# Optimization experiments

Measured on AMD Instinct MI355X. Metric: run time of the kernel, lower is better.

The kernel has to match this reference:

```python
import jax, jax.numpy as jnp
import numpy as np

EPS = 1e-5  # eqx.nn.LayerNorm default


def _layer_norm(x, w, b):
    m = x.mean(-1, keepdims=True)
    v = ((x - m) ** 2).mean(-1, keepdims=True)
    return (x - m) / jnp.sqrt(v + EPS) * w + b


def _s4_block(x, nw, nb, lre, lim, bre, bim, cre, cim, d, lstep, ow, ob, o2w, o2b):
    # x: [L, H]. One SequenceBlock: LayerNorm -> S4 recurrence (lax.scan) -> GELU -> GLU-style gated linear -> residual.
    skip = x
    h = _layer_norm(x, nw, nb)
    Lam = lre + 1j * lim                      # [H, N] complex diagonal state matrix
    step = jnp.exp(lstep)[:, None]            # [H, 1] per-channel timescale
    BL = 1.0 / (1.0 - (step / 2.0) * Lam)     # bilinear discretization
    Abar = BL * (1.0 + (step / 2.0) * Lam)    # [H, N]
    Bbar = BL * step * (bre + 1j * bim)       # [H, N]
    C = cre + 1j * cim                        # [H, N]

    def scan_fn(state, u):                    # state: [H, N] complex, u: [H]
        new = Abar * state + Bbar * u[:, None]
        y = 2.0 * jnp.sum(C * new, axis=-1).real + d * u
        return new, y

    init = jnp.zeros(Abar.shape, Abar.dtype)  # cell.init_state
    _, y = jax.lax.scan(scan_fn, init, h)     # [L, H]
    y = jax.nn.gelu(y)
    y = (y @ ow.T + ob) * jax.nn.sigmoid(y @ o2w.T + o2b)
    return skip + y


def setup_inputs() -> dict:
    key = jax.random.key(0)
    L, IN, OUT, H, N, NL = 2048, 4, 3, 512, 32, 4
    ks = jax.random.split(key, 16)
    return {
        "x": jax.random.normal(ks[0], (L, IN), jnp.float32),
        "enc_w": jax.random.normal(ks[1], (H, IN), jnp.float32) / np.sqrt(IN),
        "enc_b": jnp.zeros((H,), jnp.float32),
        "dec_w": jax.random.normal(ks[2], (OUT, H), jnp.float32) / np.sqrt(H),
        "dec_b": jnp.zeros((OUT,), jnp.float32),
        "norm_w": jnp.ones((NL, H), jnp.float32),
        "norm_b": jnp.zeros((NL, H), jnp.float32),
        "lam_re": -0.5 - jax.random.uniform(ks[3], (NL, H, N), jnp.float32),  # stable (Re < 0)
        "lam_im": np.pi * jax.random.normal(ks[4], (NL, H, N), jnp.float32),
        "b_re": jax.random.normal(ks[5], (NL, H, N), jnp.float32) / np.sqrt(N),
        "b_im": jax.random.normal(ks[6], (NL, H, N), jnp.float32) / np.sqrt(N),
        "c_re": jax.random.normal(ks[7], (NL, H, N), jnp.float32) / np.sqrt(N),
        "c_im": jax.random.normal(ks[8], (NL, H, N), jnp.float32) / np.sqrt(N),
        "d": jax.random.normal(ks[9], (NL, H), jnp.float32),
        "log_step": float(np.log(1e-3)) + float(np.log(1e-1) - np.log(1e-3)) * jax.random.uniform(ks[10], (NL, H), jnp.float32),
        "out_w": jax.random.normal(ks[11], (NL, H, H), jnp.float32) / np.sqrt(H),
        "out_b": jnp.zeros((NL, H), jnp.float32),
        "out2_w": jax.random.normal(ks[12], (NL, H, H), jnp.float32) / np.sqrt(H),
        "out2_b": jnp.zeros((NL, H), jnp.float32),
    }


def reference(x, enc_w, enc_b, dec_w, dec_b, norm_w, norm_b, lam_re, lam_im, b_re, b_im, c_re, c_im, d, log_step, out_w, out_b, out2_w, out2_b):
    h = x @ enc_w.T + enc_b                   # encoder: [L, IN] -> [L, H]
    for i in range(norm_w.shape[0]):          # fixed small n_layers loop
        h = _s4_block(h, norm_w[i], norm_b[i], lam_re[i], lam_im[i], b_re[i], b_im[i],
                      c_re[i], c_im[i], d[i], log_step[i], out_w[i], out_b[i], out2_w[i], out2_b[i])
    return h @ dec_w.T + dec_b                # decoder: [L, H] -> [L, OUT]
```

## Files before the change

### kernel.cpp

```cpp
#include <hip/hip_runtime.h>
#include <hip/hip_bf16.h>
#include <math.h>

#define LSEQ 2048
#define HD   512
#define NST  32
#define LC   32
#define NCHK 64
#define SUP  8
#define NSUP 8
#define HH   (HD * HD)

typedef __bf16 bf16;
typedef __bf16 bf16x8 __attribute__((ext_vector_type(8)));
typedef float  floatx4 __attribute__((ext_vector_type(4)));

__device__ __forceinline__ float wave_reduce_add(float v) {
#pragma unroll
    for (int m = 32; m; m >>= 1) v += __shfl_xor(v, m, 64);
    return v;
}

__device__ __forceinline__ float gelu_tanh(float x) {
    float z = 0.7978845608028654f * (x + 0.044715f * x * x * x);
    float e = __expf(2.f * z);
    float th = 1.f - 2.f / (e + 1.f);
    return 0.5f * x * (1.f + th);
}

__device__ __forceinline__ void make_ab(float lre, float lim, float step,
                                        float br0, float bi0,
                                        float& ar, float& ai, float& br, float& bi) {
    float s2 = 0.5f * step;
    float dr = 1.f - s2 * lre, di = -s2 * lim;
    float inv = 1.f / (dr * dr + di * di);
    float blr = dr * inv, bli = -di * inv;
    float nr = 1.f + s2 * lre, ni = s2 * lim;
    ar = blr * nr - bli * ni;
    ai = blr * ni + bli * nr;
    float tr = step * br0, ti = step * bi0;
    br = blr * tr - bli * ti;
    bi = blr * ti + bli * tr;
}

__global__ __launch_bounds__(256) void prep_kernel(
    const float* __restrict__ lre, const float* __restrict__ lim,
    const float* __restrict__ bre, const float* __restrict__ bim,
    const float* __restrict__ cre, const float* __restrict__ cim,
    const float* __restrict__ ls,
    float2* __restrict__ cA, float2* __restrict__ cB,
    float2* __restrict__ cC, float2* __restrict__ cAp) {
    int tid = blockIdx.x * 256 + threadIdx.x;
    int lay = tid >> 14, rem = tid & 16383;
    int ch = rem >> 5, n = rem & 31;
    int src = tid;
    float step = __expf(ls[lay * HD + ch]);
    float ar, ai, br, bi;
    make_ab(lre[src], lim[src], step, bre[src], bim[src], ar, ai, br, bi);
    float xr = ar, xi = ai;
#pragma unroll
    for (int q = 0; q < 5; ++q) { float tt = xr * xr - xi * xi; xi = 2.f * xr * xi; xr = tt; }
    int dst = (lay * NST + n) * HD + ch;
    cA[dst]  = make_float2(ar, ai);
    cB[dst]  = make_float2(br, bi);
    cC[dst]  = make_float2(2.f * cre[src], 2.f * cim[src]);
    cAp[dst] = make_float2(xr, xi);
}

__global__ __launch_bounds__(256) void cvt_kernel(
    const float* __restrict__ ow, const float* __restrict__ o2w,
    bf16* __restrict__ wb) {
    const float* src = blockIdx.y ? o2w : ow;
    bf16* dst = wb + blockIdx.y * (4 * HH);
    int i = (blockIdx.x * 256 + threadIdx.x) * 8;
    float4 a = *(const float4*)(src + i);
    float4 b = *(const float4*)(src + i + 4);
    bf16x8 o;
    o[0] = (bf16)a.x; o[1] = (bf16)a.y; o[2] = (bf16)a.z; o[3] = (bf16)a.w;
    o[4] = (bf16)b.x; o[5] = (bf16)b.y; o[6] = (bf16)b.z; o[7] = (bf16)b.w;
    *(bf16x8*)(dst + i) = o;
}

__global__ __launch_bounds__(256) void enc_kernel(
    const float* __restrict__ x, const float* __restrict__ w,
    const float* __restrict__ b, float* __restrict__ h) {
    int idx = blockIdx.x * 256 + threadIdx.x;
    int t = idx >> 9, i = idx & (HD - 1);
    float acc = b[i];
    float4 xv = *(const float4*)(x + t * 4);
    float4 wv = *(const float4*)(w + i * 4);
    acc = fmaf(xv.x, wv.x, acc);
    acc = fmaf(xv.y, wv.y, acc);
    acc = fmaf(xv.z, wv.z, acc);
    acc = fmaf(xv.w, wv.w, acc);
    h[idx] = acc;
}

__global__ __launch_bounds__(256) void ln_kernel(
    const float* __restrict__ h, float* __restrict__ hn,
    const float* __restrict__ w, const float* __restrict__ b) {
    int wv = threadIdx.x >> 6, lane = threadIdx.x & 63;
    int row = blockIdx.x * 4 + wv;
    const float* hp = h + row * HD + lane * 8;
    float v[8];
    *(float4*)(v)     = *(const float4*)(hp);
    *(float4*)(v + 4) = *(const float4*)(hp + 4);
    float s = 0.f;
#pragma unroll
    for (int e = 0; e < 8; ++e) s += v[e];
    s = wave_reduce_add(s);
    float m = s * (1.f / HD);
    float q = 0.f;
#pragma unroll
    for (int e = 0; e < 8; ++e) { float d = v[e] - m; q += d * d; }
    q = wave_reduce_add(q);
    float rstd = rsqrtf(q * (1.f / HD) + 1e-5f);
    float w8[8], b8[8];
    *(float4*)(w8)     = *(const float4*)(w + lane * 8);
    *(float4*)(w8 + 4) = *(const float4*)(w + lane * 8 + 4);
    *(float4*)(b8)     = *(const float4*)(b + lane * 8);
    *(float4*)(b8 + 4) = *(const float4*)(b + lane * 8 + 4);
    float o[8];
#pragma unroll
    for (int e = 0; e < 8; ++e)
        o[e] = (v[e] - m) * rstd * w8[e] + b8[e];
    float* op = hn + row * HD + lane * 8;
    *(float4*)op       = *(float4*)o;
    *(float4*)(op + 4) = *(float4*)(o + 4);
}

__global__ __launch_bounds__(256, 2) void p1_kernel(
    const float* __restrict__ u,
    const float2* __restrict__ cA, const float2* __restrict__ cB,
    float2* __restrict__ f, int lay) {
    __shared__ float tile[4 * LC * 16];
    int tid = threadIdx.x;
    int lane = tid & 63, w = tid >> 6;
    int chl = lane & 15;
    int ch = blockIdx.x * 16 + chl;
    int sub = lane >> 4;
    int chunk = blockIdx.y * 4 + w;
    int t0 = blockIdx.y * 4 * LC;
    const float* ub = u + (size_t)t0 * HD + blockIdx.x * 16;
#pragma unroll
    for (int r = 0; r < 8; ++r) {
        int idx = r * 256 + tid;
        tile[idx] = ub[(idx >> 4) * HD + (idx & 15)];
    }
    int cbase = (lay * NST + sub * 8) * HD + ch;
    float aR[8], aI[8], bR[8], bI[8];
#pragma unroll
    for (int j = 0; j < 8; ++j) {
        float2 t = cA[cbase + j * HD]; aR[j] = t.x; aI[j] = t.y;
        t = cB[cbase + j * HD];        bR[j] = t.x; bI[j] = t.y;
    }
    float sr[8], si[8];
#pragma unroll
    for (int j = 0; j < 8; ++j) { sr[j] = 0.f; si[j] = 0.f; }
    __syncthreads();
    const float* tp = tile + (w * LC) * 16 + chl;
#pragma unroll 4
    for (int t = 0; t < LC; ++t) {
        float uu = tp[t * 16];
#pragma unroll
        for (int j = 0; j < 8; ++j) {
            float nr = fmaf(aR[j], sr[j], fmaf(-aI[j], si[j], bR[j] * uu));
            float ni = fmaf(aI[j], sr[j], fmaf( aR[j], si[j], bI[j] * uu));
            sr[j] = nr; si[j] = ni;
        }
    }
    float2* fp = f + (chunk * NST + sub * 8) * HD + ch;
#pragma unroll
    for (int j = 0; j < 8; ++j) fp[j * HD] = make_float2(sr[j], si[j]);
}

__global__ __launch_bounds__(256) void p2a_kernel(
    float2* __restrict__ f, const float2* __restrict__ cAp, int lay) {
    int tg = blockIdx.x * 256 + threadIdx.x;
    int ch = tg & 511;
    int ns = tg >> 9;
    int n = ns & 31, sup = ns >> 5;
    float2 ap = cAp[(lay * NST + n) * HD + ch];
    float2* fp = f + ((sup * SUP) * NST + n) * HD + ch;
    float sr = 0.f, si = 0.f;
#pragma unroll
    for (int j = 0; j < SUP; ++j) {
        float2 v = fp[(size_t)j * NST * HD];
        float nr = fmaf(ap.x, sr, fmaf(-ap.y, si, v.x));
        float ni = fmaf(ap.y, sr, fmaf( ap.x, si, v.y));
        sr = nr; si = ni;
        fp[(size_t)j * NST * HD] = make_float2(sr, si);
    }
}

__global__ __launch_bounds__(256) void p2b_kernel(
    float2* __restrict__ f, const float2* __restrict__ cAp, int lay) {
    int tg = blockIdx.x * 256 + threadIdx.x;
    int ch = tg & 511, n = tg >> 9;
    float2 ap = cAp[(lay * NST + n) * HD + ch];
    float xr = ap.x, xi = ap.y;
#pragma unroll
    for (int q = 0; q < 3; ++q) { float tt = xr * xr - xi * xi; xi = 2.f * xr * xi; xr = tt; }
    float2* fp = f + ((SUP - 1) * NST + n) * HD + ch;
    const size_t stride = (size_t)SUP * NST * HD;
    float sr = 0.f, si = 0.f;
#pragma unroll
    for (int k = 0; k < NSUP; ++k) {
        float2 v = fp[k * stride];
        float nr = fmaf(xr, sr, fmaf(-xi, si, v.x));
        float ni = fmaf(xi, sr, fmaf( xr, si, v.y));
        sr = nr; si = ni;
        fp[k * stride] = make_float2(sr, si);
    }
}

__global__ __launch_bounds__(256) void p2c_kernel(
    float2* __restrict__ f, const float2* __restrict__ cAp, int lay) {
    int tg = blockIdx.x * 256 + threadIdx.x;
    int ch = tg & 511;
    int ns = tg >> 9;
    int n = ns & 31, sup = ns >> 5;
    if (sup == 0) return;
    float2 ap = cAp[(lay * NST + n) * HD + ch];
    float2 S = f[((sup * SUP - 1) * NST + n) * HD + ch];
    float2* fp = f + ((sup * SUP) * NST + n) * HD + ch;
    float wr = ap.x, wi = ap.y;
#pragma unroll
    for (int j = 0; j < SUP - 1; ++j) {
        float2 v = fp[(size_t)j * NST * HD];
        v.x += wr * S.x - wi * S.y;
        v.y += wr * S.y + wi * S.x;
        fp[(size_t)j * NST * HD] = v;
        float nwr = wr * ap.x - wi * ap.y;
        float nwi = wr * ap.y + wi * ap.x;
        wr = nwr; wi = nwi;
    }
}

__global__ __launch_bounds__(256, 2) void p3_kernel(
    const float* __restrict__ u, const float2* __restrict__ f,
    const float2* __restrict__ cA, const float2* __restrict__ cB,
    const float2* __restrict__ cC, const float* __restrict__ d_p,
    bf16* __restrict__ g, int lay) {
    __shared__ float tile[4 * LC * 16];
    int tid = threadIdx.x;
    int lane = tid & 63, w = tid >> 6;
    int chl = lane & 15;
    int ch = blockIdx.x * 16 + chl;
    int sub = lane >> 4;
    int chunk = blockIdx.y * 4 + w;
    int t0 = blockIdx.y * 4 * LC;
    const float* ub = u + (size_t)t0 * HD + blockIdx.x * 16;
#pragma unroll
    for (int r = 0; r < 8; ++r) {
        int idx = r * 256 + tid;
        tile[idx] = ub[(idx >> 4) * HD + (idx & 15)];
    }
    int cbase = (lay * NST + sub * 8) * HD + ch;
    float aR[8], aI[8], bR[8], bI[8], cR[8], cI[8];
#pragma unroll
    for (int j = 0; j < 8; ++j) {
        float2 t = cA[cbase + j * HD]; aR[j] = t.x; aI[j] = t.y;
        t = cB[cbase + j * HD];        bR[j] = t.x; bI[j] = t.y;
        t = cC[cbase + j * HD];        cR[j] = t.x; cI[j] = t.y;
    }
    float dch = d_p[lay * HD + ch];
    float sr[8], si[8];
    if (chunk > 0) {
        const float2* ip = f + ((chunk - 1) * NST + sub * 8) * HD + ch;
#pragma unroll
        for (int j = 0; j < 8; ++j) { float2 v = ip[j * HD]; sr[j] = v.x; si[j] = v.y; }
    } else {
#pragma unroll
        for (int j = 0; j < 8; ++j) { sr[j] = 0.f; si[j] = 0.f; }
    }
    __syncthreads();
    const float* tp = tile + (w * LC) * 16 + chl;
    bf16* gp = g + (size_t)chunk * LC * HD + ch;
#pragma unroll 4
    for (int t = 0; t < LC; ++t) {
        float uu = tp[t * 16];
        float p = 0.f;
#pragma unroll
        for (int j = 0; j < 8; ++j) {
            float nr = fmaf(aR[j], sr[j], fmaf(-aI[j], si[j], bR[j] * uu));
            float ni = fmaf(aI[j], sr[j], fmaf( aR[j], si[j], bI[j] * uu));
            sr[j] = nr; si[j] = ni;
            p = fmaf(cR[j], nr, fmaf(-cI[j], ni, p));
        }
        p += __shfl_xor(p, 16);
        p += __shfl_xor(p, 32);
        float y = fmaf(dch, uu, p);
        if (sub == 0) gp[t * HD] = (bf16)gelu_tanh(y);
    }
}

__global__ __launch_bounds__(256) void mm_kernel(
    const bf16* __restrict__ A,
    const bf16* __restrict__ W1,
    const bf16* __restrict__ W2,
    const float* __restrict__ bias1, const float* __restrict__ bias2,
    float* __restrict__ Hio) {
    const int w = threadIdx.x >> 6, lane = threadIdx.x & 63;
    const int wm = w >> 1, wn = w & 1;
    const int mBase = blockIdx.y * 64 + wm * 32;
    const int nBase = blockIdx.x * 64 + wn * 32;
    const int lrow = lane & 15, quad = lane >> 4;

    floatx4 acc1[2][2] = {{{0.f,0.f,0.f,0.f},{0.f,0.f,0.f,0.f}},{{0.f,0.f,0.f,0.f},{0.f,0.f,0.f,0.f}}};
    floatx4 acc2[2][2] = {{{0.f,0.f,0.f,0.f},{0.f,0.f,0.f,0.f}},{{0.f,0.f,0.f,0.f},{0.f,0.f,0.f,0.f}}};

    for (int k0 = 0; k0 < HD; k0 += 32) {
        int kk = k0 + quad * 8;
        bf16x8 a0 = *(const bf16x8*)(A + (mBase + lrow) * HD + kk);
        bf16x8 a1 = *(const bf16x8*)(A + (mBase + 16 + lrow) * HD + kk);
        bf16x8 p0 = *(const bf16x8*)(W1 + (nBase + lrow) * HD + kk);
        bf16x8 p1 = *(const bf16x8*)(W1 + (nBase + 16 + lrow) * HD + kk);
        bf16x8 q0 = *(const bf16x8*)(W2 + (nBase + lrow) * HD + kk);
        bf16x8 q1 = *(const bf16x8*)(W2 + (nBase + 16 + lrow) * HD + kk);
        acc1[0][0] = __builtin_amdgcn_mfma_f32_16x16x32_bf16(a0, p0, acc1[0][0], 0, 0, 0);
        acc1[0][1] = __builtin_amdgcn_mfma_f32_16x16x32_bf16(a0, p1, acc1[0][1], 0, 0, 0);
        acc1[1][0] = __builtin_amdgcn_mfma_f32_16x16x32_bf16(a1, p0, acc1[1][0], 0, 0, 0);
        acc1[1][1] = __builtin_amdgcn_mfma_f32_16x16x32_bf16(a1, p1, acc1[1][1], 0, 0, 0);
        acc2[0][0] = __builtin_amdgcn_mfma_f32_16x16x32_bf16(a0, q0, acc2[0][0], 0, 0, 0);
        acc2[0][1] = __builtin_amdgcn_mfma_f32_16x16x32_bf16(a0, q1, acc2[0][1], 0, 0, 0);
        acc2[1][0] = __builtin_amdgcn_mfma_f32_16x16x32_bf16(a1, q0, acc2[1][0], 0, 0, 0);
        acc2[1][1] = __builtin_amdgcn_mfma_f32_16x16x32_bf16(a1, q1, acc2[1][1], 0, 0, 0);
    }

#pragma unroll
    for (int fm = 0; fm < 2; ++fm)
#pragma unroll
        for (int fn = 0; fn < 2; ++fn) {
            int j = nBase + fn * 16 + lrow;
            float bb1 = bias1[j], bb2 = bias2[j];
#pragma unroll
            for (int r = 0; r < 4; ++r) {
                int t = mBase + fm * 16 + quad * 4 + r;
                float z1 = acc1[fm][fn][r] + bb1;
                float z2 = acc2[fm][fn][r] + bb2;
                float val = z1 / (1.f + __expf(-z2));
                Hio[t * HD + j] += val;
            }
        }
}

__global__ __launch_bounds__(192) void dec_kernel(
    const float* __restrict__ h, const float* __restrict__ w,
    const float* __restrict__ b, float* __restrict__ out) {
    int j = threadIdx.x >> 6, lane = threadIdx.x & 63;
    int t = blockIdx.x;
    const float* hp = h + t * HD + lane * 8;
    float v[8];
    *(float4*)(v)     = *(const float4*)(hp);
    *(float4*)(v + 4) = *(const float4*)(hp + 4);
    float w8[8];
    *(float4*)(w8)     = *(const float4*)(w + j * HD + lane * 8);
    *(float4*)(w8 + 4) = *(const float4*)(w + j * HD + lane * 8 + 4);
    float s = 0.f;
#pragma unroll
    for (int e = 0; e < 8; ++e) s = fmaf(v[e], w8[e], s);
    s = wave_reduce_add(s);
    if (lane == 0) out[t * 3 + j] = s + b[j];
}

extern "C" void kernel_launch(void* const* d_in, const int* in_sizes, int n_in,
                              void* d_out, int out_size, void* d_ws, size_t ws_size,
                              hipStream_t stream) {
    const float* x   = (const float*)d_in[0];
    const float* ew  = (const float*)d_in[1];
    const float* eb  = (const float*)d_in[2];
    const float* dw  = (const float*)d_in[3];
    const float* db  = (const float*)d_in[4];
    const float* nw  = (const float*)d_in[5];
    const float* nb  = (const float*)d_in[6];
    const float* lre = (const float*)d_in[7];
    const float* lim = (const float*)d_in[8];
    const float* bre = (const float*)d_in[9];
    const float* bim = (const float*)d_in[10];
    const float* cre = (const float*)d_in[11];
    const float* cim = (const float*)d_in[12];
    const float* dd  = (const float*)d_in[13];
    const float* ls  = (const float*)d_in[14];
    const float* ow  = (const float*)d_in[15];
    const float* ob  = (const float*)d_in[16];
    const float* o2w = (const float*)d_in[17];
    const float* o2b = (const float*)d_in[18];

    char* ws = (char*)d_ws;
    float*  h   = (float*)ws;
    float*  hn  = (float*)(ws + (4  << 20));
    float2* f   = (float2*)(ws + (8  << 20));
    bf16*   g   = (bf16*)(ws + (24 << 20));
    bf16*   wb  = (bf16*)(ws + (26 << 20));
    float2* cA  = (float2*)(ws + (30 << 20));
    float2* cB  = (float2*)(ws + (30 << 20) + (512 << 10));
    float2* cC  = (float2*)(ws + (31 << 20));
    float2* cAp = (float2*)(ws + (31 << 20) + (512 << 10));

    prep_kernel<<<256, 256, 0, stream>>>(lre, lim, bre, bim, cre, cim, ls, cA, cB, cC, cAp);
    cvt_kernel<<<dim3(4 * HH / (256 * 8), 2), 256, 0, stream>>>(ow, o2w, wb);
    enc_kernel<<<LSEQ * HD / 256, 256, 0, stream>>>(x, ew, eb, h);
    for (int lay = 0; lay < 4; ++lay) {
        int oH = lay * HD;
        ln_kernel<<<LSEQ / 4, 256, 0, stream>>>(h, hn, nw + oH, nb + oH);
        p1_kernel<<<dim3(HD / 16, NCHK / 4), 256, 0, stream>>>(hn, cA, cB, f, lay);
        p2a_kernel<<<512, 256, 0, stream>>>(f, cAp, lay);
        p2b_kernel<<<64, 256, 0, stream>>>(f, cAp, lay);
        p2c_kernel<<<512, 256, 0, stream>>>(f, cAp, lay);
        p3_kernel<<<dim3(HD / 16, NCHK / 4), 256, 0, stream>>>(hn, f, cA, cB, cC, dd, g, lay);
        mm_kernel<<<dim3(HD / 64, LSEQ / 64), 256, 0, stream>>>(
            g, wb + lay * HH, wb + 4 * HH + lay * HH, ob + oH, o2b + oH, h);
    }
    dec_kernel<<<LSEQ, 192, 0, stream>>>(h, dw, db, (float*)d_out);
}
```

Before: 315.2 us.

## Fuse setup kernels, fold LayerNorm into scan, use wave-shuffle chunk prefix

Merges the prep, weight-convert and encoder kernels into a single setup launch. The standalone LayerNorm kernel is removed: per-row sum and sum-of-squares are accumulated with atomics in the encoder and matmul epilogues, and normalization is applied on the fly in p1/p3. The three-kernel chunk-state propagation is replaced by one wave-level shuffle prefix scan over 64 chunks. This cuts launches and removes the normalized-activation buffer round-trip. In exchange it adds atomics and a one-pass variance (E[x^2]-m^2), which is less numerically robust.

```diff
diff --git a/kernel.cpp b/kernel.cpp
--- a/kernel.cpp
+++ b/kernel.cpp
@@ -7,8 +7,6 @@
 #define NST  32
 #define LC   32
 #define NCHK 64
-#define SUP  8
-#define NSUP 8
 #define HH   (HD * HD)
 
 typedef __bf16 bf16;
@@ -43,97 +41,74 @@
     bi = blr * ti + bli * tr;
 }
 
-__global__ __launch_bounds__(256) void prep_kernel(
+__global__ __launch_bounds__(256) void setup_kernel(
+    const float* __restrict__ x,   const float* __restrict__ ew,
+    const float* __restrict__ eb,
     const float* __restrict__ lre, const float* __restrict__ lim,
     const float* __restrict__ bre, const float* __restrict__ bim,
     const float* __restrict__ cre, const float* __restrict__ cim,
-    const float* __restrict__ ls,
+    const float* __restrict__ ls,  const float* __restrict__ ow,
+    const float* __restrict__ o2w,
+    float* __restrict__ h, bf16* __restrict__ wb,
     float2* __restrict__ cA, float2* __restrict__ cB,
-    float2* __restrict__ cC, float2* __restrict__ cAp) {
-    int tid = blockIdx.x * 256 + threadIdx.x;
-    int lay = tid >> 14, rem = tid & 16383;
-    int ch = rem >> 5, n = rem & 31;
-    int src = tid;
-    float step = __expf(ls[lay * HD + ch]);
-    float ar, ai, br, bi;
-    make_ab(lre[src], lim[src], step, bre[src], bim[src], ar, ai, br, bi);
-    float xr = ar, xi = ai;
-#pragma unroll
-    for (int q = 0; q < 5; ++q) { float tt = xr * xr - xi * xi; xi = 2.f * xr * xi; xr = tt; }
-    int dst = (lay * NST + n) * HD + ch;
-    cA[dst]  = make_float2(ar, ai);
-    cB[dst]  = make_float2(br, bi);
-    cC[dst]  = make_float2(2.f * cre[src], 2.f * cim[src]);
-    cAp[dst] = make_float2(xr, xi);
-}
-
-__global__ __launch_bounds__(256) void cvt_kernel(
-    const float* __restrict__ ow, const float* __restrict__ o2w,
-    bf16* __restrict__ wb) {
-    const float* src = blockIdx.y ? o2w : ow;
-    bf16* dst = wb + blockIdx.y * (4 * HH);
-    int i = (blockIdx.x * 256 + threadIdx.x) * 8;
-    float4 a = *(const float4*)(src + i);
-    float4 b = *(const float4*)(src + i + 4);
-    bf16x8 o;
-    o[0] = (bf16)a.x; o[1] = (bf16)a.y; o[2] = (bf16)a.z; o[3] = (bf16)a.w;
-    o[4] = (bf16)b.x; o[5] = (bf16)b.y; o[6] = (bf16)b.z; o[7] = (bf16)b.w;
-    *(bf16x8*)(dst + i) = o;
-}
-
-__global__ __launch_bounds__(256) void enc_kernel(
-    const float* __restrict__ x, const float* __restrict__ w,
-    const float* __restrict__ b, float* __restrict__ h) {
-    int idx = blockIdx.x * 256 + threadIdx.x;
-    int t = idx >> 9, i = idx & (HD - 1);
-    float acc = b[i];
-    float4 xv = *(const float4*)(x + t * 4);
-    float4 wv = *(const float4*)(w + i * 4);
-    acc = fmaf(xv.x, wv.x, acc);
-    acc = fmaf(xv.y, wv.y, acc);
-    acc = fmaf(xv.z, wv.z, acc);
-    acc = fmaf(xv.w, wv.w, acc);
-    h[idx] = acc;
-}
-
-__global__ __launch_bounds__(256) void ln_kernel(
-    const float* __restrict__ h, float* __restrict__ hn,
-    const float* __restrict__ w, const float* __restrict__ b) {
-    int wv = threadIdx.x >> 6, lane = threadIdx.x & 63;
-    int row = blockIdx.x * 4 + wv;
-    const float* hp = h + row * HD + lane * 8;
-    float v[8];
-    *(float4*)(v)     = *(const float4*)(hp);
-    *(float4*)(v + 4) = *(const float4*)(hp + 4);
-    float s = 0.f;
-#pragma unroll
-    for (int e = 0; e < 8; ++e) s += v[e];
-    s = wave_reduce_add(s);
-    float m = s * (1.f / HD);
-    float q = 0.f;
-#pragma unroll
-    for (int e = 0; e < 8; ++e) { float d = v[e] - m; q += d * d; }
-    q = wave_reduce_add(q);
-    float rstd = rsqrtf(q * (1.f / HD) + 1e-5f);
-    float w8[8], b8[8];
-    *(float4*)(w8)     = *(const float4*)(w + lane * 8);
-    *(float4*)(w8 + 4) = *(const float4*)(w + lane * 8 + 4);
-    *(float4*)(b8)     = *(const float4*)(b + lane * 8);
-    *(float4*)(b8 + 4) = *(const float4*)(b + lane * 8 + 4);
-    float o[8];
-#pragma unroll
-    for (int e = 0; e < 8; ++e)
-        o[e] = (v[e] - m) * rstd * w8[e] + b8[e];
-    float* op = hn + row * HD + lane * 8;
-    *(float4*)op       = *(float4*)o;
-    *(float4*)(op + 4) = *(float4*)(o + 4);
+    float2* __restrict__ cC, float2* __restrict__ cAp,
+    float* __restrict__ st0)
+{
+    int bid = blockIdx.x, tid = threadIdx.x;
+    if (bid < 256) {
+        int tg = bid * 256 + tid;
+        int lay = tg >> 14, rem = tg & 16383;
+        int ch = rem >> 5, n = rem & 31;
+        float step = __expf(ls[lay * HD + ch]);
+        float ar, ai, br, bi;
+        make_ab(lre[tg], lim[tg], step, bre[tg], bim[tg], ar, ai, br, bi);
+        float xr = ar, xi = ai;
+#pragma unroll
+        for (int q = 0; q < 5; ++q) { float tt = xr * xr - xi * xi; xi = 2.f * xr * xi; xr = tt; }
+        int dst = (lay * NST + n) * HD + ch;
+        cA[dst]  = make_float2(ar, ai);
+        cB[dst]  = make_float2(br, bi);
+        cC[dst]  = make_float2(2.f * cre[tg], 2.f * cim[tg]);
+        cAp[dst] = make_float2(xr, xi);
+    } else if (bid < 768) {
+        int i = ((bid - 256) * 256 + tid) * 8;
+        float4 a = *(const float4*)(ow + i);
+        float4 b = *(const float4*)(ow + i + 4);
+        bf16x8 o;
+        o[0]=(bf16)a.x; o[1]=(bf16)a.y; o[2]=(bf16)a.z; o[3]=(bf16)a.w;
+        o[4]=(bf16)b.x; o[5]=(bf16)b.y; o[6]=(bf16)b.z; o[7]=(bf16)b.w;
+        *(bf16x8*)(wb + i) = o;
+        a = *(const float4*)(o2w + i);
+        b = *(const float4*)(o2w + i + 4);
+        o[0]=(bf16)a.x; o[1]=(bf16)a.y; o[2]=(bf16)a.z; o[3]=(bf16)a.w;
+        o[4]=(bf16)b.x; o[5]=(bf16)b.y; o[6]=(bf16)b.z; o[7]=(bf16)b.w;
+        *(bf16x8*)(wb + 4 * HH + i) = o;
+    } else {
+        int i = (bid - 768) * 256 + tid;
+        int t = i >> 9, c = i & 511;
+        float4 xv = *(const float4*)(x + t * 4);
+        float4 wv = *(const float4*)(ew + c * 4);
+        float acc = eb[c];
+        acc = fmaf(xv.x, wv.x, acc); acc = fmaf(xv.y, wv.y, acc);
+        acc = fmaf(xv.z, wv.z, acc); acc = fmaf(xv.w, wv.w, acc);
+        h[i] = acc;
+        float s1 = wave_reduce_add(acc);
+        float s2 = wave_reduce_add(acc * acc);
+        if ((tid & 63) == 0) {
+            atomicAdd(&st0[t * 2],     s1);
+            atomicAdd(&st0[t * 2 + 1], s2);
+        }
+    }
 }
 
 __global__ __launch_bounds__(256, 2) void p1_kernel(
-    const float* __restrict__ u,
+    const float* __restrict__ h, const float* __restrict__ st,
     const float2* __restrict__ cA, const float2* __restrict__ cB,
+    const float* __restrict__ nw, const float* __restrict__ nb,
     float2* __restrict__ f, int lay) {
-    __shared__ float tile[4 * LC * 16];
+    __shared__ float  tile[4 * LC * 16];
+    __shared__ float2 sml[128];
+    __shared__ float  snw[16], snb[16];
     int tid = threadIdx.x;
     int lane = tid & 63, w = tid >> 6;
     int chl = lane & 15;
@@ -141,12 +116,22 @@
     int sub = lane >> 4;
     int chunk = blockIdx.y * 4 + w;
     int t0 = blockIdx.y * 4 * LC;
-    const float* ub = u + (size_t)t0 * HD + blockIdx.x * 16;
+    const float* ub = h + (size_t)t0 * HD + blockIdx.x * 16;
 #pragma unroll
     for (int r = 0; r < 8; ++r) {
         int idx = r * 256 + tid;
         tile[idx] = ub[(idx >> 4) * HD + (idx & 15)];
     }
+    if (tid < 128) {
+        float s1 = st[(t0 + tid) * 2], s2 = st[(t0 + tid) * 2 + 1];
+        float m = s1 * (1.f / HD);
+        float var = s2 * (1.f / HD) - m * m;
+        sml[tid] = make_float2(m, rsqrtf(var + 1e-5f));
+    }
+    if (tid < 16) {
+        snw[tid] = nw[lay * HD + blockIdx.x * 16 + tid];
+        snb[tid] = nb[lay * HD + blockIdx.x * 16 + tid];
+    }
     int cbase = (lay * NST + sub * 8) * HD + ch;
     float aR[8], aI[8], bR[8], bI[8];
 #pragma unroll
@@ -158,10 +143,12 @@
 #pragma unroll
     for (int j = 0; j < 8; ++j) { sr[j] = 0.f; si[j] = 0.f; }
     __syncthreads();
-    const float* tp = tile + (w * LC) * 16 + chl;
+    float wch = snw[chl], bch = snb[chl];
 #pragma unroll 4
     for (int t = 0; t < LC; ++t) {
-        float uu = tp[t * 16];
+        int row = w * LC + t;
+        float2 ms = sml[row];
+        float uu = (tile[row * 16 + chl] - ms.x) * ms.y * wch + bch;
 #pragma unroll
         for (int j = 0; j < 8; ++j) {
             float nr = fmaf(aR[j], sr[j], fmaf(-aI[j], si[j], bR[j] * uu));
@@ -169,80 +156,47 @@
             sr[j] = nr; si[j] = ni;
         }
     }
-    float2* fp = f + (chunk * NST + sub * 8) * HD + ch;
+    float2* fp = f + ((size_t)chunk * NST + sub * 8) * HD + ch;
 #pragma unroll
     for (int j = 0; j < 8; ++j) fp[j * HD] = make_float2(sr[j], si[j]);
 }
 
-__global__ __launch_bounds__(256) void p2a_kernel(
+__global__ __launch_bounds__(256) void p2_kernel(
     float2* __restrict__ f, const float2* __restrict__ cAp, int lay) {
-    int tg = blockIdx.x * 256 + threadIdx.x;
-    int ch = tg & 511;
-    int ns = tg >> 9;
-    int n = ns & 31, sup = ns >> 5;
+    int w = threadIdx.x >> 6, lane = threadIdx.x & 63;
+    int chain = blockIdx.x * 4 + w;
+    int ch = chain & 511, n = chain >> 9;
     float2 ap = cAp[(lay * NST + n) * HD + ch];
-    float2* fp = f + ((sup * SUP) * NST + n) * HD + ch;
-    float sr = 0.f, si = 0.f;
-#pragma unroll
-    for (int j = 0; j < SUP; ++j) {
-        float2 v = fp[(size_t)j * NST * HD];
-        float nr = fmaf(ap.x, sr, fmaf(-ap.y, si, v.x));
-        float ni = fmaf(ap.y, sr, fmaf( ap.x, si, v.y));
-        sr = nr; si = ni;
-        fp[(size_t)j * NST * HD] = make_float2(sr, si);
-    }
-}
-
-__global__ __launch_bounds__(256) void p2b_kernel(
-    float2* __restrict__ f, const float2* __restrict__ cAp, int lay) {
-    int tg = blockIdx.x * 256 + threadIdx.x;
-    int ch = tg & 511, n = tg >> 9;
-    float2 ap = cAp[(lay * NST + n) * HD + ch];
-    float xr = ap.x, xi = ap.y;
-#pragma unroll
-    for (int q = 0; q < 3; ++q) { float tt = xr * xr - xi * xi; xi = 2.f * xr * xi; xr = tt; }
-    float2* fp = f + ((SUP - 1) * NST + n) * HD + ch;
-    const size_t stride = (size_t)SUP * NST * HD;
-    float sr = 0.f, si = 0.f;
-#pragma unroll
-    for (int k = 0; k < NSUP; ++k) {
-        float2 v = fp[k * stride];
-        float nr = fmaf(xr, sr, fmaf(-xi, si, v.x));
-        float ni = fmaf(xi, sr, fmaf( xr, si, v.y));
-        sr = nr; si = ni;
-        fp[k * stride] = make_float2(sr, si);
-    }
-}
-
-__global__ __launch_bounds__(256) void p2c_kernel(
-    float2* __restrict__ f, const float2* __restrict__ cAp, int lay) {
-    int tg = blockIdx.x * 256 + threadIdx.x;
-    int ch = tg & 511;
-    int ns = tg >> 9;
-    int n = ns & 31, sup = ns >> 5;
-    if (sup == 0) return;
-    float2 ap = cAp[(lay * NST + n) * HD + ch];
-    float2 S = f[((sup * SUP - 1) * NST + n) * HD + ch];
-    float2* fp = f + ((sup * SUP) * NST + n) * HD + ch;
-    float wr = ap.x, wi = ap.y;
-#pragma unroll
-    for (int j = 0; j < SUP - 1; ++j) {
-        float2 v = fp[(size_t)j * NST * HD];
-        v.x += wr * S.x - wi * S.y;
-        v.y += wr * S.y + wi * S.x;
-        fp[(size_t)j * NST * HD] = v;
-        float nwr = wr * ap.x - wi * ap.y;
-        float nwi = wr * ap.y + wi * ap.x;
-        wr = nwr; wi = nwi;
-    }
+    size_t idx = ((size_t)lane * NST + n) * HD + ch;
+    float2 v = f[idx];
+    float vr = v.x, vi = v.y, wr = ap.x, wi = ap.y;
+#pragma unroll
+    for (int d = 1; d < 64; d <<= 1) {
+        float pvr = __shfl_up(vr, d, 64);
+        float pvi = __shfl_up(vi, d, 64);
+        float pwr = __shfl_up(wr, d, 64);
+        float pwi = __shfl_up(wi, d, 64);
+        if (lane >= d) {
+            vr += wr * pvr - wi * pvi;
+            vi += wr * pvi + wi * pvr;
+            float nr = wr * pwr - wi * pwi;
+            float ni = wr * pwi + wi * pwr;
+            wr = nr; wi = ni;
+        }
+    }
+    f[idx] = make_float2(vr, vi);
 }
 
 __global__ __launch_bounds__(256, 2) void p3_kernel(
-    const float* __restrict__ u, const float2* __restrict__ f,
+    const float* __restrict__ h, const float* __restrict__ st,
+    const float2* __restrict__ f,
     const float2* __restrict__ cA, const float2* __restrict__ cB,
-    const float2* __restrict__ cC, const float* __restrict__ d_p,
+    const float2* __restrict__ cC, const float* __restrict__ dd,
+    const float* __restrict__ nw, const float* __restrict__ nb,
     bf16* __restrict__ g, int lay) {
-    __shared__ float tile[4 * LC * 16];
+    __shared__ float  tile[4 * LC * 16];
+    __shared__ float2 sml[128];
+    __shared__ float  snw[16], snb[16];
     int tid = threadIdx.x;
     int lane = tid & 63, w = tid >> 6;
     int chl = lane & 15;
@@ -250,11 +204,21 @@
     int sub = lane >> 4;
     int chunk = blockIdx.y * 4 + w;
     int t0 = blockIdx.y * 4 * LC;
-    const float* ub = u + (size_t)t0 * HD + blockIdx.x * 16;
+    const float* ub = h + (size_t)t0 * HD + blockIdx.x * 16;
 #pragma unroll
     for (int r = 0; r < 8; ++r) {
         int idx = r * 256 + tid;
         tile[idx] = ub[(idx >> 4) * HD + (idx & 15)];
+    }
+    if (tid < 128) {
+        float s1 = st[(t0 + tid) * 2], s2 = st[(t0 + tid) * 2 + 1];
+        float m = s1 * (1.f / HD);
+        float var = s2 * (1.f / HD) - m * m;
+        sml[tid] = make_float2(m, rsqrtf(var + 1e-5f));
+    }
+    if (tid < 16) {
+        snw[tid] = nw[lay * HD + blockIdx.x * 16 + tid];
+        snb[tid] = nb[lay * HD + blockIdx.x * 16 + tid];
     }
     int cbase = (lay * NST + sub * 8) * HD + ch;
     float aR[8], aI[8], bR[8], bI[8], cR[8], cI[8];
@@ -264,10 +228,10 @@
         t = cB[cbase + j * HD];        bR[j] = t.x; bI[j] = t.y;
         t = cC[cbase + j * HD];        cR[j] = t.x; cI[j] = t.y;
     }
-    float dch = d_p[lay * HD + ch];
+    float dch = dd[lay * HD + ch];
     float sr[8], si[8];
     if (chunk > 0) {
-        const float2* ip = f + ((chunk - 1) * NST + sub * 8) * HD + ch;
+        const float2* ip = f + ((size_t)(chunk - 1) * NST + sub * 8) * HD + ch;
 #pragma unroll
         for (int j = 0; j < 8; ++j) { float2 v = ip[j * HD]; sr[j] = v.x; si[j] = v.y; }
     } else {
@@ -275,11 +239,13 @@
         for (int j = 0; j < 8; ++j) { sr[j] = 0.f; si[j] = 0.f; }
     }
     __syncthreads();
-    const float* tp = tile + (w * LC) * 16 + chl;
+    float wch = snw[chl], bch = snb[chl];
     bf16* gp = g + (size_t)chunk * LC * HD + ch;
 #pragma unroll 4
     for (int t = 0; t < LC; ++t) {
-        float uu = tp[t * 16];
+        int row = w * LC + t;
+        float2 ms = sml[row];
+        float uu = (tile[row * 16 + chl] - ms.x) * ms.y * wch + bch;
         float p = 0.f;
 #pragma unroll
         for (int j = 0; j < 8; ++j) {
@@ -300,7 +266,7 @@
     const bf16* __restrict__ W1,
     const bf16* __restrict__ W2,
     const float* __restrict__ bias1, const float* __restrict__ bias2,
-    float* __restrict__ Hio) {
+    float* __restrict__ Hio, float* __restrict__ stn) {
     const int w = threadIdx.x >> 6, lane = threadIdx.x & 63;
     const int wm = w >> 1, wn = w & 1;
     const int mBase = blockIdx.y * 64 + wm * 32;
@@ -328,6 +294,7 @@
         acc2[1][1] = __builtin_amdgcn_mfma_f32_16x16x32_bf16(a1, q1, acc2[1][1], 0, 0, 0);
     }
 
+    float hv[2][2][4];
 #pragma unroll
     for (int fm = 0; fm < 2; ++fm)
 #pragma unroll
@@ -339,8 +306,26 @@
                 int t = mBase + fm * 16 + quad * 4 + r;
                 float z1 = acc1[fm][fn][r] + bb1;
                 float z2 = acc2[fm][fn][r] + bb2;
-                float val = z1 / (1.f + __expf(-z2));
-                Hio[t * HD + j] += val;
+                float nv = Hio[t * HD + j] + z1 / (1.f + __expf(-z2));
+                Hio[t * HD + j] = nv;
+                hv[fm][fn][r] = nv;
+            }
+        }
+#pragma unroll
+    for (int fm = 0; fm < 2; ++fm)
+#pragma unroll
+        for (int r = 0; r < 4; ++r) {
+            int t = mBase + fm * 16 + quad * 4 + r;
+            float s1 = hv[fm][0][r] + hv[fm][1][r];
+            float s2 = hv[fm][0][r] * hv[fm][0][r] + hv[fm][1][r] * hv[fm][1][r];
+#pragma unroll
+            for (int m = 1; m < 16; m <<= 1) {
+                s1 += __shfl_xor(s1, m);
+                s2 += __shfl_xor(s2, m);
+            }
+            if (lrow == 0) {
+                atomicAdd(&stn[t * 2],     s1);
+                atomicAdd(&stn[t * 2 + 1], s2);
             }
         }
 }
@@ -386,31 +371,31 @@
     const float* ob  = (const float*)d_in[16];
     const float* o2w = (const float*)d_in[17];
     const float* o2b = (const float*)d_in[18];
-
     char* ws = (char*)d_ws;
-    float*  h   = (float*)ws;
-    float*  hn  = (float*)(ws + (4  << 20));
-    float2* f   = (float2*)(ws + (8  << 20));
-    bf16*   g   = (bf16*)(ws + (24 << 20));
-    bf16*   wb  = (bf16*)(ws + (26 << 20));
-    float2* cA  = (float2*)(ws + (30 << 20));
-    float2* cB  = (float2*)(ws + (30 << 20) + (512 << 10));
-    float2* cC  = (float2*)(ws + (31 << 20));
-    float2* cAp = (float2*)(ws + (31 << 20) + (512 << 10));
-
-    prep_kernel<<<256, 256, 0, stream>>>(lre, lim, bre, bim, cre, cim, ls, cA, cB, cC, cAp);
-    cvt_kernel<<<dim3(4 * HH / (256 * 8), 2), 256, 0, stream>>>(ow, o2w, wb);
-    enc_kernel<<<LSEQ * HD / 256, 256, 0, stream>>>(x, ew, eb, h);
+
+    float*  h     = (float*)ws;
+    float2* f     = (float2*)(ws + (4  << 20));
+    bf16*   g     = (bf16*)(ws + (12 << 20));
+    bf16*   wb    = (bf16*)(ws + (14 << 20));
+    float*  stats = (float*)(ws + (18 << 20));
+    float2* cA    = (float2*)(ws + (19 << 20));
+    float2* cB    = cA + 4 * NST * HD;
+    float2* cC    = cB + 4 * NST * HD;
+    float2* cAp   = cC + 4 * NST * HD;
+
+    hipMemsetAsync(stats, 0, 5 * LSEQ * 2 * sizeof(float), stream);
+    setup_kernel<<<4864, 256, 0, stream>>>(x, ew, eb, lre, lim, bre, bim,
+                                           cre, cim, ls, ow, o2w,
+                                           h, wb, cA, cB, cC, cAp, stats);
     for (int lay = 0; lay < 4; ++lay) {
-        int oH = lay * HD;
-        ln_kernel<<<LSEQ / 4, 256, 0, stream>>>(h, hn, nw + oH, nb + oH);
-        p1_kernel<<<dim3(HD / 16, NCHK / 4), 256, 0, stream>>>(hn, cA, cB, f, lay);
-        p2a_kernel<<<512, 256, 0, stream>>>(f, cAp, lay);
-        p2b_kernel<<<64, 256, 0, stream>>>(f, cAp, lay);
-        p2c_kernel<<<512, 256, 0, stream>>>(f, cAp, lay);
-        p3_kernel<<<dim3(HD / 16, NCHK / 4), 256, 0, stream>>>(hn, f, cA, cB, cC, dd, g, lay);
-        mm_kernel<<<dim3(HD / 64, LSEQ / 64), 256, 0, stream>>>(
-            g, wb + lay * HH, wb + 4 * HH + lay * HH, ob + oH, o2b + oH, h);
+        float* st  = stats + lay * LSEQ * 2;
+        float* stn = stats + (lay + 1) * LSEQ * 2;
+        p1_kernel<<<dim3(32, 16), 256, 0, stream>>>(h, st, cA, cB, nw, nb, f, lay);
+        p2_kernel<<<4096, 256, 0, stream>>>(f, cAp, lay);
+        p3_kernel<<<dim3(32, 16), 256, 0, stream>>>(h, st, f, cA, cB, cC, dd, nw, nb, g, lay);
+        mm_kernel<<<dim3(8, 32), 256, 0, stream>>>(
+            g, wb + lay * HH, wb + 4 * HH + lay * HH,
+            ob + lay * HD, o2b + lay * HD, h, stn);
     }
     dec_kernel<<<LSEQ, 192, 0, stream>>>(h, dw, db, (float*)d_out);
 }
```

After: 362.9 us. +15.1%, slower.
